# Kernel optimization log

Measured on AMD Instinct MI355X. Metric: run time of the kernel, lower is better.

## Reference

```python
import jax, jax.numpy as jnp
import numpy as np

B, T, K = 512, 512, 64


def setup_inputs() -> dict:
    key = jax.random.key(0)
    k1, k2, k3, k4, k5 = jax.random.split(key, 5)
    emissions = jax.random.normal(k1, (B, T, K), dtype=jnp.float32)
    tags = jax.random.randint(k2, (B, T), 0, K)
    mask = jnp.ones((B, T), dtype=bool)  # torchcrf requires mask[:, 0] to be on
    # torchcrf initializes CRF params ~ U(-0.1, 0.1)
    start_transitions = jax.random.uniform(k3, (K,), minval=-0.1, maxval=0.1, dtype=jnp.float32)
    end_transitions = jax.random.uniform(k4, (K,), minval=-0.1, maxval=0.1, dtype=jnp.float32)
    transitions = jax.random.uniform(k5, (K, K), minval=-0.1, maxval=0.1, dtype=jnp.float32)
    return {"emissions": emissions, "tags": tags, "mask": mask,
            "start_transitions": start_transitions,
            "end_transitions": end_transitions,
            "transitions": transitions}


def _crf_nll(emissions, tags, mask, start_transitions, end_transitions, transitions):
    # emissions [B,T,K], tags [B,T] int, mask [B,T] bool
    b, t, k = emissions.shape
    maskf = mask.astype(emissions.dtype)
    batch = jnp.arange(b)

    # ---- numerator: score of the gold tag sequence ----
    em = jnp.take_along_axis(emissions, tags[:, :, None], axis=2)[:, :, 0]  # [B,T]
    score = start_transitions[tags[:, 0]] + em[:, 0]
    tr_sc = transitions[tags[:, :-1], tags[:, 1:]]  # [B,T-1]
    score = score + jnp.sum((tr_sc + em[:, 1:]) * maskf[:, 1:], axis=1)
    seq_ends = jnp.sum(mask.astype(jnp.int32), axis=1) - 1  # [B]
    last_tags = tags[batch, seq_ends]
    score = score + end_transitions[last_tags]

    # ---- denominator: log-partition via forward algorithm (scan over time) ----
    alpha0 = start_transitions[None, :] + emissions[:, 0]  # [B,K]

    def step(alpha, inp):
        em_t, m_t = inp  # [B,K], [B]
        # [B, prev K, next K] -> logsumexp over prev
        nxt = jax.nn.logsumexp(alpha[:, :, None] + transitions[None, :, :] + em_t[:, None, :], axis=1)
        alpha = jnp.where(m_t[:, None], nxt, alpha)
        return alpha, None

    em_rest = jnp.swapaxes(emissions[:, 1:], 0, 1)  # [T-1,B,K]
    m_rest = jnp.swapaxes(mask[:, 1:], 0, 1)        # [T-1,B]
    alphaT, _ = jax.lax.scan(step, alpha0, (em_rest, m_rest))
    denom = jax.nn.logsumexp(alphaT + end_transitions[None, :], axis=1)  # [B]

    llh = score - denom  # [B]
    return -jnp.mean(llh)  # reduction='mean', loss = -llh


def reference(emissions, tags, mask, start_transitions, end_transitions, transitions):
    return _crf_nll(emissions, tags, mask, start_transitions, end_transitions, transitions)
```

## Files before the change

### kernel.cpp

```cpp
#include <hip/hip_runtime.h>

#define KK 64
#define TT 512
#define BB 512


typedef float f32x16 __attribute__((ext_vector_type(16)));

__device__ __forceinline__ float bcast(unsigned bits) { return __uint_as_float(bits); }

__global__ __launch_bounds__(64) void crf_score(
    const float* __restrict__ em, const int* __restrict__ tags,
    const float* __restrict__ start, const float* __restrict__ endt,
    const float* __restrict__ trans, float* __restrict__ score_out)
{
  const int b = blockIdx.x;
  const int lane = threadIdx.x;
  const int* tg = tags + b * TT;
  const float* e = em + (size_t)b * TT * KK;
  float s = 0.f;
#pragma unroll
  for (int rep = 0; rep < TT / 64; ++rep) {
    int t = rep * 64 + lane;
    int cur = tg[t];
    s += e[t * KK + cur];
    if (t > 0) s += trans[tg[t - 1] * KK + cur];
  }
#pragma unroll
  for (int off = 32; off; off >>= 1) s += __shfl_xor(s, off);
  if (lane == 0) {
    s += start[tg[0]] + endt[tg[TT - 1]];
    score_out[b] = s;
  }
}

__global__ __launch_bounds__(64, 1) void crf_forward(
    const float* __restrict__ em, const float* __restrict__ start,
    const float* __restrict__ endt, const float* __restrict__ trans,
    float* __restrict__ denom_out)
{
  const int b = blockIdx.x;
  const int j = threadIdx.x;
  const float LOG2E = 1.44269504088896340736f;
  const float LN2 = 0.69314718055994530942f;

  f32x16 E0, E1, E2, E3;
#pragma unroll
  for (int i = 0; i < 16; ++i) {
    E0[i] = exp2f(trans[(i)      * KK + j] * LOG2E);
    E1[i] = exp2f(trans[(i + 16) * KK + j] * LOG2E);
    E2[i] = exp2f(trans[(i + 32) * KK + j] * LOG2E);
    E3[i] = exp2f(trans[(i + 48) * KK + j] * LOG2E);
  }
  const float Eend = exp2f(endt[j] * LOG2E);

  const float* ep = em + (size_t)b * TT * KK + j;
  float v = exp2f((start[j] + ep[0]) * LOG2E);
  float S2 = 0.f;

  float emA = ep[KK];
  float emB = ep[2 * KK];

  for (int t = 1; t < TT; ++t) {
    float w = exp2f(emA * LOG2E);
    emA = emB;
    int tn = (t + 2 < TT) ? t + 2 : TT - 1;
    emB = ep[tn * KK];

    unsigned vb = __float_as_uint(v);
    float a0 = 0.f, a1 = 0.f, a2 = 0.f, a3 = 0.f;
#pragma unroll
    for (int i = 0; i < 16; ++i) {
      a0 = fmaf(bcast(__builtin_amdgcn_readlane(vb, i)),      E0[i], a0);
      a1 = fmaf(bcast(__builtin_amdgcn_readlane(vb, i + 16)), E1[i], a1);
      a2 = fmaf(bcast(__builtin_amdgcn_readlane(vb, i + 32)), E2[i], a2);
      a3 = fmaf(bcast(__builtin_amdgcn_readlane(vb, i + 48)), E3[i], a3);
    }
    v = ((a0 + a1) + (a2 + a3)) * w;

    if ((t & 7) == 0) {
      float m = v;
#pragma unroll
      for (int off = 32; off; off >>= 1) m = fmaxf(m, __shfl_xor(m, off));
      S2 += log2f(m);
      v *= (1.0f / m);
    }
  }

  float acc = v * Eend;
#pragma unroll
  for (int off = 32; off; off >>= 1) acc += __shfl_xor(acc, off);
  if (j == 0) denom_out[b] = (log2f(acc) + S2) * LN2;
}

__global__ __launch_bounds__(512) void crf_final(
    const float* __restrict__ score, const float* __restrict__ denom,
    float* __restrict__ out)
{
  const int i = threadIdx.x;
  float d = denom[i] - score[i];
  __shared__ float red[8];
#pragma unroll
  for (int off = 32; off; off >>= 1) d += __shfl_xor(d, off);
  if ((i & 63) == 0) red[i >> 6] = d;
  __syncthreads();
  if (i == 0) {
    float s = 0.f;
#pragma unroll
    for (int wv = 0; wv < 8; ++wv) s += red[wv];
    out[0] = s / (float)BB;
  }
}

extern "C" void kernel_launch(void* const* d_in, const int* in_sizes, int n_in,
                              void* d_out, int out_size, void* d_ws, size_t ws_size,
                              hipStream_t stream) {
  const float* em    = (const float*)d_in[0];
  const int*   tags  = (const int*)d_in[1];
  const float* start = (const float*)d_in[3];
  const float* endt  = (const float*)d_in[4];
  const float* trans = (const float*)d_in[5];

  float* score = (float*)d_ws;
  float* denom = score + BB;

  crf_score<<<BB, 64, 0, stream>>>(em, tags, start, endt, trans, score);
  crf_forward<<<BB, 64, 0, stream>>>(em, start, endt, trans, denom);
  crf_final<<<1, BB, 0, stream>>>(score, denom, (float*)d_out);
}
```

Measured before the change: 173.0 us.

## Run the CRF forward recursion as batched bf16 MFMA matvecs over 32 sequences

Replaces the one-wave-per-sequence readlane/FMA forward recursion with one wave per 32 sequences. Each step is computed as a 64x64 by 64x32 bf16 MFMA product, and the state is repacked with cvt_pk_bf16 and permlane32 swaps. A separate kernel optionally precomputes exp(emissions) into a workspace table in the MFMA fragment layout. Renormalization uses exponent extraction every third step, and emission loads are triple-buffered. This is meant to cut per-step scalar latency and instruction count, but it launches only 16 workgroups and lowers precision to bf16 for the state and transition exponentials.

```diff
diff --git a/kernel.cpp b/kernel.cpp
--- a/kernel.cpp
+++ b/kernel.cpp
@@ -3,11 +3,14 @@
 #define KK 64
 #define TT 512
 #define BB 512
-
+#define NW (BB / 32)
+#define LOG2E 1.44269504088896340736f
+#define LN2 0.69314718055994530942f
 
 typedef float f32x16 __attribute__((ext_vector_type(16)));
-
-__device__ __forceinline__ float bcast(unsigned bits) { return __uint_as_float(bits); }
+typedef float f32x4v __attribute__((ext_vector_type(4)));
+typedef int i32x4 __attribute__((ext_vector_type(4)));
+typedef short bf16x8 __attribute__((ext_vector_type(8)));
 
 __global__ __launch_bounds__(64) void crf_score(
     const float* __restrict__ em, const int* __restrict__ tags,
@@ -34,63 +37,169 @@
   }
 }
 
-__global__ __launch_bounds__(64, 1) void crf_forward(
-    const float* __restrict__ em, const float* __restrict__ start,
-    const float* __restrict__ endt, const float* __restrict__ trans,
-    float* __restrict__ denom_out)
-{
-  const int b = blockIdx.x;
-  const int j = threadIdx.x;
-  const float LOG2E = 1.44269504088896340736f;
-  const float LN2 = 0.69314718055994530942f;
-
-  f32x16 E0, E1, E2, E3;
-#pragma unroll
-  for (int i = 0; i < 16; ++i) {
-    E0[i] = exp2f(trans[(i)      * KK + j] * LOG2E);
-    E1[i] = exp2f(trans[(i + 16) * KK + j] * LOG2E);
-    E2[i] = exp2f(trans[(i + 32) * KK + j] * LOG2E);
-    E3[i] = exp2f(trans[(i + 48) * KK + j] * LOG2E);
-  }
-  const float Eend = exp2f(endt[j] * LOG2E);
-
-  const float* ep = em + (size_t)b * TT * KK + j;
-  float v = exp2f((start[j] + ep[0]) * LOG2E);
+__global__ __launch_bounds__(256) void crf_wexp(const float* __restrict__ em,
+                                                float* __restrict__ wout)
+{
+  int tid = blockIdx.x * 256 + threadIdx.x;
+  int l = tid & 63;
+  int i = (tid >> 6) & 7;
+  int t = (tid >> 9) & 511;
+  int cw = tid >> 18;
+  int b = cw * 32 + (l & 31);
+  int jb = (i >> 2) * 32 + (i & 3) * 8 + (l >> 5) * 4;
+  f32x4v e = *(const f32x4v*)(em + ((size_t)b * TT + t) * KK + jb);
+  f32x4v w;
+  w[0] = exp2f(e[0] * LOG2E);
+  w[1] = exp2f(e[1] * LOG2E);
+  w[2] = exp2f(e[2] * LOG2E);
+  w[3] = exp2f(e[3] * LOG2E);
+  ((f32x4v*)wout)[tid] = w;
+}
+
+
+#define XR(kt, q) ((kt) < 2 ? x0[((kt)&1) * 8 + (q)] : x1[((kt)&1) * 8 + (q)])
+
+#define LOADW(WBUF, TN)                                                        \
+  {                                                                            \
+    int tn_ = (TN) < TT ? (TN) : (TT - 1);                                     \
+    if (USEW) {                                                                \
+      _Pragma("unroll") for (int i2 = 0; i2 < 8; ++i2)                         \
+          WBUF[i2] = wb_base[((size_t)tn_ * 8 + i2) * 64 + lane];              \
+    } else {                                                                   \
+      _Pragma("unroll") for (int i2 = 0; i2 < 8; ++i2)                         \
+          WBUF[i2] = *(const f32x4v*)(em_b + (size_t)tn_ * KK +                \
+                                      (i2 >> 2) * 32 + (i2 & 3) * 8 + hi * 4);\
+    }                                                                          \
+  }
+
+#define STEP(WBUF, TNEXT, RENORM)                                              \
+  {                                                                            \
+    f32x16 d0 = {};                                                            \
+    f32x16 d1 = {};                                                            \
+    _Pragma("unroll") for (int kt = 0; kt < 4; ++kt)                           \
+    {                                                                          \
+      bf16x8 bfv = __builtin_bit_cast(bf16x8, st[kt]);                         \
+      d0 = __builtin_amdgcn_mfma_f32_32x32x16_bf16(afr[0][kt], bfv, d0, 0, 0, 0);\
+      d1 = __builtin_amdgcn_mfma_f32_32x32x16_bf16(afr[1][kt], bfv, d1, 0, 0, 0);\
+    }                                                                          \
+    f32x16 x0, x1;                                                             \
+    if (USEW) {                                                                \
+      _Pragma("unroll") for (int q = 0; q < 16; ++q)                           \
+      {                                                                        \
+        x0[q] = d0[q] * WBUF[q >> 2][q & 3];                                   \
+        x1[q] = d1[q] * WBUF[4 + (q >> 2)][q & 3];                             \
+      }                                                                        \
+    } else {                                                                   \
+      _Pragma("unroll") for (int q = 0; q < 16; ++q)                           \
+      {                                                                        \
+        x0[q] = d0[q] * exp2f(WBUF[q >> 2][q & 3] * LOG2E);                    \
+        x1[q] = d1[q] * exp2f(WBUF[4 + (q >> 2)][q & 3] * LOG2E);              \
+      }                                                                        \
+    }                                                                          \
+    if (RENORM) {                                                              \
+      float m_ = x0[0];                                                        \
+      float px_ = m_, py_ = m_;                                                \
+      asm("v_permlane32_swap_b32 %0, %1" : "+v"(px_), "+v"(py_));              \
+      float pm_ = (lane & 32) ? py_ : px_;                                     \
+      float mm_ = fmaxf(m_, pm_);                                              \
+      int ee_ = (int)(__float_as_uint(mm_) >> 23) - 127;                       \
+      S2 += (float)ee_;                                                        \
+      _Pragma("unroll") for (int q = 0; q < 16; ++q)                           \
+      {                                                                        \
+        x0[q] = ldexpf(x0[q], -ee_);                                           \
+        x1[q] = ldexpf(x1[q], -ee_);                                           \
+      }                                                                        \
+    }                                                                          \
+    LOADW(WBUF, TNEXT)                                                         \
+    _Pragma("unroll") for (int kt = 0; kt < 4; ++kt)                           \
+    {                                                                          \
+      int P0, P1, P2, P3;                                                      \
+      asm("v_cvt_pk_bf16_f32 %0, %1, %2" : "=v"(P0) : "v"(XR(kt, 0)), "v"(XR(kt, 1)));\
+      asm("v_cvt_pk_bf16_f32 %0, %1, %2" : "=v"(P1) : "v"(XR(kt, 2)), "v"(XR(kt, 3)));\
+      asm("v_cvt_pk_bf16_f32 %0, %1, %2" : "=v"(P2) : "v"(XR(kt, 4)), "v"(XR(kt, 5)));\
+      asm("v_cvt_pk_bf16_f32 %0, %1, %2" : "=v"(P3) : "v"(XR(kt, 6)), "v"(XR(kt, 7)));\
+      asm("v_permlane32_swap_b32 %0, %1" : "+v"(P2), "+v"(P0));                \
+      asm("v_permlane32_swap_b32 %0, %1" : "+v"(P3), "+v"(P1));                \
+      st[kt] = (i32x4){P0, P1, P2, P3};                                        \
+    }                                                                          \
+  }
+
+template <bool USEW>
+__global__ __attribute__((amdgpu_flat_work_group_size(64, 64),
+                          amdgpu_waves_per_eu(1, 1)))
+void crf_forward_mfma(const float* __restrict__ em,
+                      const float* __restrict__ start,
+                      const float* __restrict__ endt,
+                      const float* __restrict__ trans,
+                      const float* __restrict__ wtab,
+                      float* __restrict__ denom_out)
+{
+  const int cw = blockIdx.x;
+  const int lane = threadIdx.x;
+  const int lo = lane & 31;
+  const int hi = lane >> 5;
+  const int b = cw * 32 + lo;
+  const float* em_b = em + (size_t)b * TT * KK;
+  const f32x4v* wb_base = (const f32x4v*)wtab + (size_t)cw * TT * 8 * 64;
+
+  bf16x8 afr[2][4];
+#pragma unroll
+  for (int rt = 0; rt < 2; ++rt)
+#pragma unroll
+    for (int kt = 0; kt < 4; ++kt) {
+      int pw[4];
+#pragma unroll
+      for (int p = 0; p < 4; ++p) {
+        int k0 = kt * 16 + hi * 8 + 2 * p;
+        float e0 = exp2f(trans[k0 * KK + rt * 32 + lo] * LOG2E);
+        float e1 = exp2f(trans[(k0 + 1) * KK + rt * 32 + lo] * LOG2E);
+        asm("v_cvt_pk_bf16_f32 %0, %1, %2" : "=v"(pw[p]) : "v"(e0), "v"(e1));
+      }
+      afr[rt][kt] = __builtin_bit_cast(bf16x8, (i32x4){pw[0], pw[1], pw[2], pw[3]});
+    }
+
+  i32x4 st[4];
+#pragma unroll
+  for (int kt = 0; kt < 4; ++kt) {
+    int pw[4];
+#pragma unroll
+    for (int p = 0; p < 4; ++p) {
+      int j0 = kt * 16 + hi * 8 + 2 * p;
+      float v0 = exp2f((start[j0] + em_b[j0]) * LOG2E);
+      float v1 = exp2f((start[j0 + 1] + em_b[j0 + 1]) * LOG2E);
+      asm("v_cvt_pk_bf16_f32 %0, %1, %2" : "=v"(pw[p]) : "v"(v0), "v"(v1));
+    }
+    st[kt] = (i32x4){pw[0], pw[1], pw[2], pw[3]};
+  }
+
   float S2 = 0.f;
-
-  float emA = ep[KK];
-  float emB = ep[2 * KK];
-
-  for (int t = 1; t < TT; ++t) {
-    float w = exp2f(emA * LOG2E);
-    emA = emB;
-    int tn = (t + 2 < TT) ? t + 2 : TT - 1;
-    emB = ep[tn * KK];
-
-    unsigned vb = __float_as_uint(v);
-    float a0 = 0.f, a1 = 0.f, a2 = 0.f, a3 = 0.f;
-#pragma unroll
-    for (int i = 0; i < 16; ++i) {
-      a0 = fmaf(bcast(__builtin_amdgcn_readlane(vb, i)),      E0[i], a0);
-      a1 = fmaf(bcast(__builtin_amdgcn_readlane(vb, i + 16)), E1[i], a1);
-      a2 = fmaf(bcast(__builtin_amdgcn_readlane(vb, i + 32)), E2[i], a2);
-      a3 = fmaf(bcast(__builtin_amdgcn_readlane(vb, i + 48)), E3[i], a3);
+  f32x4v wA[8], wB[8], wC[8];
+  LOADW(wA, 1)
+  LOADW(wB, 2)
+  LOADW(wC, 3)
+
+  int tb = 1;
+  for (int it = 0; it < 170; ++it) {
+    STEP(wA, tb + 3, false)
+    STEP(wB, tb + 4, false)
+    STEP(wC, tb + 5, true)
+    tb += 3;
+  }
+  STEP(wA, TT - 1, false)
+
+  float sum = 0.f;
+#pragma unroll
+  for (int kt = 0; kt < 4; ++kt)
+#pragma unroll
+    for (int f = 0; f < 4; ++f) {
+      int w = st[kt][f];
+      int j0 = kt * 16 + hi * 8 + 2 * f;
+      float vlo = __uint_as_float(((unsigned)w) << 16);
+      float vhi = __uint_as_float(((unsigned)w) & 0xffff0000u);
+      sum += vlo * exp2f(endt[j0] * LOG2E) + vhi * exp2f(endt[j0 + 1] * LOG2E);
     }
-    v = ((a0 + a1) + (a2 + a3)) * w;
-
-    if ((t & 7) == 0) {
-      float m = v;
-#pragma unroll
-      for (int off = 32; off; off >>= 1) m = fmaxf(m, __shfl_xor(m, off));
-      S2 += log2f(m);
-      v *= (1.0f / m);
-    }
-  }
-
-  float acc = v * Eend;
-#pragma unroll
-  for (int off = 32; off; off >>= 1) acc += __shfl_xor(acc, off);
-  if (j == 0) denom_out[b] = (log2f(acc) + S2) * LN2;
+  float total = sum + __shfl_xor(sum, 32);
+  if (lane < 32) denom_out[cw * 32 + lane] = (log2f(total) + S2) * LN2;
 }
 
 __global__ __launch_bounds__(512) void crf_final(
@@ -115,16 +224,23 @@
 extern "C" void kernel_launch(void* const* d_in, const int* in_sizes, int n_in,
                               void* d_out, int out_size, void* d_ws, size_t ws_size,
                               hipStream_t stream) {
-  const float* em    = (const float*)d_in[0];
-  const int*   tags  = (const int*)d_in[1];
+  const float* em = (const float*)d_in[0];
+  const int* tags = (const int*)d_in[1];
   const float* start = (const float*)d_in[3];
-  const float* endt  = (const float*)d_in[4];
+  const float* endt = (const float*)d_in[4];
   const float* trans = (const float*)d_in[5];
 
   float* score = (float*)d_ws;
   float* denom = score + BB;
+  float* wtab = (float*)((char*)d_ws + 8192);
+  const size_t wbytes = (size_t)NW * TT * 8 * 64 * 16;
 
   crf_score<<<BB, 64, 0, stream>>>(em, tags, start, endt, trans, score);
-  crf_forward<<<BB, 64, 0, stream>>>(em, start, endt, trans, denom);
+  if (ws_size >= 8192 + wbytes) {
+    crf_wexp<<<(NW * TT * 8 * 64) / 256, 256, 0, stream>>>(em, wtab);
+    crf_forward_mfma<true><<<NW, 64, 0, stream>>>(em, start, endt, trans, wtab, denom);
+  } else {
+    crf_forward_mfma<false><<<NW, 64, 0, stream>>>(em, start, endt, trans, nullptr, denom);
+  }
   crf_final<<<1, BB, 0, stream>>>(score, denom, (float*)d_out);
 }
```

Result: slower. 198.6 us (+14.8%).
